# Kernel tuning notes

Hardware: AMD Instinct MI355X
Metric: run time of the kernel (lower is better)

Reference implementation:

```python
import jax, jax.numpy as jnp
import numpy as np

FL = 320       # frame length
FS = 80        # frame shift
ORDER = 16     # poly order (a[0] == 1)
EMPH = 0.97    # pre/de-emphasis coefficient


def setup_inputs() -> dict:
    key = jax.random.key(0)
    k1, k2 = jax.random.split(key)
    B, F = 64, 3000
    L = F * FS  # 240000
    excit = jax.random.normal(k1, (B, L, 1), dtype=jnp.float32) * 0.1
    # LPC coefficients: a[0] = 1, remaining taps small for numerical stability
    rest = jax.random.normal(k2, (B, F, ORDER - 1), dtype=jnp.float32) * (0.3 / (ORDER - 1))
    lpc_coef = jnp.concatenate([jnp.ones((B, F, 1), jnp.float32), rest], axis=-1)
    return {"excit": excit, "lpc_coef": lpc_coef}


def reference(excit, lpc_coef):
    """LPCSynthesisPytorch: AR synthesis recursion followed by de-emphasis.

    excit:    (B, L, 1)
    lpc_coef: (B, F, order), a[0] assumed 1, L = F * FS
    returns:  (B, L, 1)
    """
    B, L, _ = excit.shape
    order = lpc_coef.shape[-1]

    # Per-sample AR taps a[1:], expanded frame->sample, time-major for scan.
    a = jnp.repeat(lpc_coef[:, :, 1:], FS, axis=1)[:, :L]      # (B, L, order-1)
    a_t = jnp.transpose(a, (1, 0, 2))                          # (L, B, order-1)
    e_t = jnp.transpose(excit[..., 0], (1, 0))                 # (L, B)

    def ar_step(buf, inp):
        # buf: (B, order-1) = [x[n-order+1], ..., x[n-1]] (last entry most recent)
        a_n, e_n = inp
        # predicted = sum_k a[k] * x[n-k]; output = excit - predicted
        pre = -jnp.sum(a_n * buf[:, ::-1], axis=-1)
        out = e_n + pre
        buf = jnp.concatenate([buf[:, 1:], out[:, None]], axis=-1)
        return buf, out

    buf0 = jnp.zeros((B, order - 1), dtype=excit.dtype)
    _, y_t = jax.lax.scan(ar_step, buf0, (a_t, e_t))           # (L, B)

    # De-emphasis IIR: z[n] = y[n] + EMPH * z[n-1], z[-1] = 0
    def deemph_step(prev, x):
        cur = x + EMPH * prev
        return cur, cur

    _, z_t = jax.lax.scan(deemph_step, jnp.zeros((B,), excit.dtype), y_t)
    return jnp.transpose(z_t, (1, 0))[..., None]               # (B, L, 1)
```

## Files before the change

### kernel.cpp

```cpp
#include <hip/hip_runtime.h>


namespace {
constexpr int kFS = 80;
constexpr int kHS = 40;
constexpr int kF = 3000;
constexpr int kH = 2 * kF;
constexpr int kL = kFS * kF;
constexpr int kOrder = 16;
constexpr int kB = 64;
constexpr float kEmph = 0.97f;
constexpr int kThreads = 128;
constexpr int kJunk = 9;
constexpr int kEmitH = kThreads - kJunk;
constexpr int kSlotF = 44;
constexpr int kBufF = kThreads * kSlotF;
constexpr int kIss = kBufF / (2 * 64 * 4);
constexpr int kNT = 3;
constexpr int kCols = 17;
constexpr float kLg97 = -4.3943347e-2f;
constexpr float kR1 = 0.2957118f;
constexpr float kR2 = 0.08744547f;
constexpr float kR3 = 0.02585867f;
constexpr float kR4 = 0.00764671f;
constexpr float kR5 = 0.00226126f;
constexpr float kR6 = 6.6867e-4f;
constexpr float kR7 = 1.9773e-4f;
constexpr float kR8 = 5.8472e-5f;

typedef float vfloat4 __attribute__((ext_vector_type(4)));

__device__ __forceinline__ void stage_tile(const float* __restrict__ ebase,
                                           float* sbuf, int tile, int wv,
                                           int ln) {
#pragma unroll
  for (int i = 0; i < kIss; ++i) {
    const int c = wv * kIss + i;
    const int W4 = c * 64 + ln;
    const int s = W4 / 11;
    const int o4 = W4 - s * 11;
    const int ht = tile * kEmitH + s - kJunk;
    const int hc = min(max(ht, 0), kH - 1);
    const int fidx = min(hc * kHS + o4 * 4, kL - 4);
    __builtin_amdgcn_global_load_lds(
        (const __attribute__((address_space(1))) float*)(ebase + fidx),
        (__attribute__((address_space(3))) float*)(sbuf + (c << 8)), 16, 0,
        0);
  }
}
}

#define AR_SAMPLE(A, s, e_in, ACC)                                         \
  float ACC;                                                               \
  {                                                                        \
    float t0 = (e_in);                                                     \
    t0 = fmaf(-A[14], x[((s)-15) & 15], t0);                               \
    t0 = fmaf(-A[13], x[((s)-14) & 15], t0);                               \
    t0 = fmaf(-A[12], x[((s)-13) & 15], t0);                               \
    t0 = fmaf(-A[11], x[((s)-12) & 15], t0);                               \
    t0 = fmaf(-A[10], x[((s)-11) & 15], t0);                               \
    float t1 = -A[9] * x[((s)-10) & 15];                                   \
    t1 = fmaf(-A[8], x[((s)-9) & 15], t1);                                 \
    t1 = fmaf(-A[7], x[((s)-8) & 15], t1);                                 \
    t1 = fmaf(-A[6], x[((s)-7) & 15], t1);                                 \
    t1 = fmaf(-A[5], x[((s)-6) & 15], t1);                                 \
    float t2 = -A[4] * x[((s)-5) & 15];                                    \
    t2 = fmaf(-A[3], x[((s)-4) & 15], t2);                                 \
    t2 = fmaf(-A[2], x[((s)-3) & 15], t2);                                 \
    t2 = fmaf(-A[1], x[((s)-2) & 15], t2);                                 \
    const float t01 = t0 + t1;                      \
    t2 = fmaf(-A[0], x[((s)-1) & 15], t2);            \
    ACC = t01 + t2;                                           \
    x[(s)&15] = ACC;                                                       \
  }

__global__ __launch_bounds__(kThreads) void lpc_synth_kernel(
    const float* __restrict__ excit, const float* __restrict__ coef,
    float* __restrict__ out) {
  __shared__ float s_ex[2 * kBufF];
  __shared__ float s_zend[kThreads];
  __shared__ float s_zp[kThreads];

  const int tid = threadIdx.x;
  const int ln = tid & 63;
  const int wv = tid >> 6;
  const int b = blockIdx.y;
  const int tile0 = blockIdx.x * kNT;

  const float* __restrict__ ebase = excit + (size_t)b * kL;
  const float* __restrict__ cbase = coef + (size_t)b * kF * kOrder;
  float* __restrict__ outb = out + (size_t)b * kL;

  stage_tile(ebase, s_ex, tile0, wv, ln);

#pragma unroll 1
  for (int t = 0; t < kNT; ++t) {
    const int tile = tile0 + t;
    float* __restrict__ sb = s_ex + (t & 1) * kBufF;
    float* __restrict__ sn = s_ex + ((t + 1) & 1) * kBufF;

    __syncthreads();

    if (t + 1 < kNT) {
      stage_tile(ebase, sn, tile + 1, wv, ln);
      __builtin_amdgcn_sched_barrier(0);
    }

    const int ht = tile * kEmitH + tid - kJunk;
    const int hc = min(max(ht, 0), kH - 1);
    const int hw = min(max(ht - 2, 0), kH - 1);

    const vfloat4* __restrict__ cp_ =
        (const vfloat4*)(cbase + (size_t)(hw >> 1) * kOrder);
    const vfloat4* __restrict__ cc_ =
        (const vfloat4*)(cbase + (size_t)(hc >> 1) * kOrder);
    const vfloat4 p0 = cp_[0], p1 = cp_[1], p2 = cp_[2], p3 = cp_[3];
    const vfloat4 q0 = cc_[0], q1 = cc_[1], q2 = cc_[2], q3 = cc_[3];

    float x[16];
#pragma unroll
    for (int i = 0; i < 16; ++i) x[i] = 0.f;
    float pa_[15] = {p0.y, p0.z, p0.w, p1.x, p1.y, p1.z, p1.w, p2.x,
                     p2.y, p2.z, p2.w, p3.x, p3.y, p3.z, p3.w};
    const float ca_[15] = {q0.y, q0.z, q0.w, q1.x, q1.y, q1.z, q1.w, q2.x,
                           q2.y, q2.z, q2.w, q3.x, q3.y, q3.z, q3.w};
    {
      const float* __restrict__ s2 = sb + max(tid - 2, 0) * kSlotF;
      const float* __restrict__ s1 = sb + max(tid - 1, 0) * kSlotF;
      const float m2 = (ht >= 2) ? 1.f : 0.f;
      const float m1 = (ht >= 1) ? 1.f : 0.f;
#pragma unroll
      for (int j = 8; j < 10; ++j) {
        const vfloat4 v = *(const vfloat4*)(s2 + 4 * j);
        const float f_[4] = {m2 * v.x, m2 * v.y, m2 * v.z, m2 * v.w};
#pragma unroll
        for (int q = 0; q < 4; ++q) {
          AR_SAMPLE(pa_, 4 * (j - 8) + q, f_[q], acc)
          (void)acc;
        }
      }
      if (ht & 1) {
#pragma unroll
        for (int k = 0; k < 15; ++k) pa_[k] = ca_[k];
      }
#pragma unroll
      for (int j = 0; j < 10; ++j) {
        const vfloat4 v = *(const vfloat4*)(s1 + 4 * j);
        const float f_[4] = {m1 * v.x, m1 * v.y, m1 * v.z, m1 * v.w};
#pragma unroll
        for (int q = 0; q < 4; ++q) {
          AR_SAMPLE(pa_, 8 + 4 * j + q, f_[q], acc)
          (void)acc;
        }
      }
    }
    __syncthreads();

    float z = 0.f;
    {
      float* __restrict__ so = sb + tid * kSlotF;
#pragma unroll
      for (int j = 0; j < 10; ++j) {
        const vfloat4 v = *(const vfloat4*)(so + 4 * j);
        vfloat4 zv;
#pragma unroll
        for (int q = 0; q < 4; ++q) {
          AR_SAMPLE(ca_, 48 + 4 * j + q, v[q], acc)
          z = fmaf(kEmph, z, acc);
          if (q == 0) zv.x = z;
          if (q == 1) zv.y = z;
          if (q == 2) zv.z = z;
          if (q == 3) zv.w = z;
        }
        *(vfloat4*)(so + 4 * j) = zv;
      }
    }
    s_zend[tid] = (ht < 0 || ht >= kH) ? 0.f : z;
    __syncthreads();

    if (tid < kEmitH) {
      float Zp = s_zend[tid + 8];
      Zp = fmaf(kR1, s_zend[tid + 7], Zp);
      Zp = fmaf(kR2, s_zend[tid + 6], Zp);
      Zp = fmaf(kR3, s_zend[tid + 5], Zp);
      Zp = fmaf(kR4, s_zend[tid + 4], Zp);
      Zp = fmaf(kR5, s_zend[tid + 3], Zp);
      Zp = fmaf(kR6, s_zend[tid + 2], Zp);
      Zp = fmaf(kR7, s_zend[tid + 1], Zp);
      Zp = fmaf(kR8, s_zend[tid + 0], Zp);
      s_zp[tid] = Zp;
    }
    __syncthreads();

    {
      const int hbase = tile * kEmitH;
      const int nv4 = min(kEmitH, kH - hbase) * 10;
      vfloat4* __restrict__ ob = (vfloat4*)(outb + (size_t)hbase * kHS);
#pragma unroll 1
      for (int i = tid; i < nv4; i += kThreads) {
        const int k = i / 10;
        const int j = i - 10 * k;
        const vfloat4 h =
            *(const vfloat4*)(sb + (k + kJunk) * kSlotF + 4 * j);
        const float Zp = s_zp[k];
        const float ee = __builtin_exp2f(kLg97 * (float)(4 * j + 1));
        vfloat4 v;
        v.x = fmaf(ee, Zp, h.x);
        v.y = fmaf(ee * 0.97f, Zp, h.y);
        v.z = fmaf(ee * 0.9409f, Zp, h.z);
        v.w = fmaf(ee * 0.912673f, Zp, h.w);
        ob[i] = v;
      }
    }
  }
}
#undef AR_SAMPLE

extern "C" void kernel_launch(void* const* d_in, const int* in_sizes, int n_in,
                              void* d_out, int out_size, void* d_ws,
                              size_t ws_size, hipStream_t stream) {
  const float* excit = (const float*)d_in[0];
  const float* coef = (const float*)d_in[1];
  float* out = (float*)d_out;

  dim3 grid(kCols, kB);
  lpc_synth_kernel<<<grid, kThreads, 0, stream>>>(excit, coef, out);
}
```

Before: 139.5 us.

## Drop LDS staging and multi-tile loop; read excitation directly from global

Removes the double-buffered global_load_lds staging of excitation and the three-tile-per-block loop. Each thread now loads its own half-frames straight from global memory (three overlapping reads per thread), and the grid is tripled so each block processes one tile. LDS shrinks to a z-only buffer with a 42-float slot, accessed with float2 ops. This trades the async prefetch overlap for more blocks, higher occupancy and fewer barriers, at the cost of redundant global reads that rely on the cache.

```diff
diff --git a/kernel.cpp b/kernel.cpp
--- a/kernel.cpp
+++ b/kernel.cpp
@@ -2,22 +2,18 @@
 
 
 namespace {
-constexpr int kFS = 80;
 constexpr int kHS = 40;
 constexpr int kF = 3000;
 constexpr int kH = 2 * kF;
-constexpr int kL = kFS * kF;
+constexpr int kL = kHS * kH;
 constexpr int kOrder = 16;
 constexpr int kB = 64;
 constexpr float kEmph = 0.97f;
 constexpr int kThreads = 128;
 constexpr int kJunk = 9;
 constexpr int kEmitH = kThreads - kJunk;
-constexpr int kSlotF = 44;
-constexpr int kBufF = kThreads * kSlotF;
-constexpr int kIss = kBufF / (2 * 64 * 4);
-constexpr int kNT = 3;
-constexpr int kCols = 17;
+constexpr int kSlotF = 42;
+constexpr int kCols = 51;
 constexpr float kLg97 = -4.3943347e-2f;
 constexpr float kR1 = 0.2957118f;
 constexpr float kR2 = 0.08744547f;
@@ -29,25 +25,7 @@
 constexpr float kR8 = 5.8472e-5f;
 
 typedef float vfloat4 __attribute__((ext_vector_type(4)));
-
-__device__ __forceinline__ void stage_tile(const float* __restrict__ ebase,
-                                           float* sbuf, int tile, int wv,
-                                           int ln) {
-#pragma unroll
-  for (int i = 0; i < kIss; ++i) {
-    const int c = wv * kIss + i;
-    const int W4 = c * 64 + ln;
-    const int s = W4 / 11;
-    const int o4 = W4 - s * 11;
-    const int ht = tile * kEmitH + s - kJunk;
-    const int hc = min(max(ht, 0), kH - 1);
-    const int fidx = min(hc * kHS + o4 * 4, kL - 4);
-    __builtin_amdgcn_global_load_lds(
-        (const __attribute__((address_space(1))) float*)(ebase + fidx),
-        (__attribute__((address_space(3))) float*)(sbuf + (c << 8)), 16, 0,
-        0);
-  }
-}
+typedef float vfloat2 __attribute__((ext_vector_type(2)));
 }
 
 #define AR_SAMPLE(A, s, e_in, ACC)                                         \
@@ -77,140 +55,125 @@
 __global__ __launch_bounds__(kThreads) void lpc_synth_kernel(
     const float* __restrict__ excit, const float* __restrict__ coef,
     float* __restrict__ out) {
-  __shared__ float s_ex[2 * kBufF];
+  __shared__ float s_z[kThreads * kSlotF];
   __shared__ float s_zend[kThreads];
   __shared__ float s_zp[kThreads];
 
   const int tid = threadIdx.x;
-  const int ln = tid & 63;
-  const int wv = tid >> 6;
   const int b = blockIdx.y;
-  const int tile0 = blockIdx.x * kNT;
+  const int hbase = blockIdx.x * kEmitH;
+  const int ht = hbase + tid - kJunk;
+  const int hc = min(max(ht, 0), kH - 1);
+  const int h1 = min(max(ht - 1, 0), kH - 1);
+  const int h2 = min(max(ht - 2, 0), kH - 1);
 
   const float* __restrict__ ebase = excit + (size_t)b * kL;
   const float* __restrict__ cbase = coef + (size_t)b * kF * kOrder;
-  float* __restrict__ outb = out + (size_t)b * kL;
 
-  stage_tile(ebase, s_ex, tile0, wv, ln);
+  const vfloat4* __restrict__ cp_ =
+      (const vfloat4*)(cbase + (size_t)(h2 >> 1) * kOrder);
+  const vfloat4* __restrict__ cc_ =
+      (const vfloat4*)(cbase + (size_t)(hc >> 1) * kOrder);
+  const vfloat4 p0 = cp_[0], p1 = cp_[1], p2 = cp_[2], p3 = cp_[3];
+  const vfloat4 q0 = cc_[0], q1 = cc_[1], q2 = cc_[2], q3 = cc_[3];
 
-#pragma unroll 1
-  for (int t = 0; t < kNT; ++t) {
-    const int tile = tile0 + t;
-    float* __restrict__ sb = s_ex + (t & 1) * kBufF;
-    float* __restrict__ sn = s_ex + ((t + 1) & 1) * kBufF;
+  float pa_[15] = {p0.y, p0.z, p0.w, p1.x, p1.y, p1.z, p1.w, p2.x,
+                   p2.y, p2.z, p2.w, p3.x, p3.y, p3.z, p3.w};
+  const float ca_[15] = {q0.y, q0.z, q0.w, q1.x, q1.y, q1.z, q1.w, q2.x,
+                         q2.y, q2.z, q2.w, q3.x, q3.y, q3.z, q3.w};
 
-    __syncthreads();
+  float x[16];
+#pragma unroll
+  for (int i = 0; i < 16; ++i) x[i] = 0.f;
 
-    if (t + 1 < kNT) {
-      stage_tile(ebase, sn, tile + 1, wv, ln);
-      __builtin_amdgcn_sched_barrier(0);
-    }
-
-    const int ht = tile * kEmitH + tid - kJunk;
-    const int hc = min(max(ht, 0), kH - 1);
-    const int hw = min(max(ht - 2, 0), kH - 1);
-
-    const vfloat4* __restrict__ cp_ =
-        (const vfloat4*)(cbase + (size_t)(hw >> 1) * kOrder);
-    const vfloat4* __restrict__ cc_ =
-        (const vfloat4*)(cbase + (size_t)(hc >> 1) * kOrder);
-    const vfloat4 p0 = cp_[0], p1 = cp_[1], p2 = cp_[2], p3 = cp_[3];
-    const vfloat4 q0 = cc_[0], q1 = cc_[1], q2 = cc_[2], q3 = cc_[3];
-
-    float x[16];
+  {
+    const vfloat4* __restrict__ e2 = (const vfloat4*)(ebase + h2 * kHS);
+    const vfloat4* __restrict__ e1 = (const vfloat4*)(ebase + h1 * kHS);
+    const float m2 = (ht >= 2) ? 1.f : 0.f;
+    const float m1 = (ht >= 1) ? 1.f : 0.f;
 #pragma unroll
-    for (int i = 0; i < 16; ++i) x[i] = 0.f;
-    float pa_[15] = {p0.y, p0.z, p0.w, p1.x, p1.y, p1.z, p1.w, p2.x,
-                     p2.y, p2.z, p2.w, p3.x, p3.y, p3.z, p3.w};
-    const float ca_[15] = {q0.y, q0.z, q0.w, q1.x, q1.y, q1.z, q1.w, q2.x,
-                           q2.y, q2.z, q2.w, q3.x, q3.y, q3.z, q3.w};
-    {
-      const float* __restrict__ s2 = sb + max(tid - 2, 0) * kSlotF;
-      const float* __restrict__ s1 = sb + max(tid - 1, 0) * kSlotF;
-      const float m2 = (ht >= 2) ? 1.f : 0.f;
-      const float m1 = (ht >= 1) ? 1.f : 0.f;
+    for (int j = 8; j < 10; ++j) {
+      const vfloat4 v = e2[j];
+      const float f_[4] = {m2 * v.x, m2 * v.y, m2 * v.z, m2 * v.w};
 #pragma unroll
-      for (int j = 8; j < 10; ++j) {
-        const vfloat4 v = *(const vfloat4*)(s2 + 4 * j);
-        const float f_[4] = {m2 * v.x, m2 * v.y, m2 * v.z, m2 * v.w};
-#pragma unroll
-        for (int q = 0; q < 4; ++q) {
-          AR_SAMPLE(pa_, 4 * (j - 8) + q, f_[q], acc)
-          (void)acc;
-        }
-      }
-      if (ht & 1) {
-#pragma unroll
-        for (int k = 0; k < 15; ++k) pa_[k] = ca_[k];
-      }
-#pragma unroll
-      for (int j = 0; j < 10; ++j) {
-        const vfloat4 v = *(const vfloat4*)(s1 + 4 * j);
-        const float f_[4] = {m1 * v.x, m1 * v.y, m1 * v.z, m1 * v.w};
-#pragma unroll
-        for (int q = 0; q < 4; ++q) {
-          AR_SAMPLE(pa_, 8 + 4 * j + q, f_[q], acc)
-          (void)acc;
-        }
+      for (int q = 0; q < 4; ++q) {
+        AR_SAMPLE(pa_, 4 * (j - 8) + q, f_[q], acc)
+        (void)acc;
       }
     }
-    __syncthreads();
-
-    float z = 0.f;
-    {
-      float* __restrict__ so = sb + tid * kSlotF;
+    if (ht & 1) {
 #pragma unroll
-      for (int j = 0; j < 10; ++j) {
-        const vfloat4 v = *(const vfloat4*)(so + 4 * j);
-        vfloat4 zv;
+      for (int k = 0; k < 15; ++k) pa_[k] = ca_[k];
+    }
 #pragma unroll
-        for (int q = 0; q < 4; ++q) {
-          AR_SAMPLE(ca_, 48 + 4 * j + q, v[q], acc)
-          z = fmaf(kEmph, z, acc);
-          if (q == 0) zv.x = z;
-          if (q == 1) zv.y = z;
-          if (q == 2) zv.z = z;
-          if (q == 3) zv.w = z;
-        }
-        *(vfloat4*)(so + 4 * j) = zv;
+    for (int j = 0; j < 10; ++j) {
+      const vfloat4 v = e1[j];
+      const float f_[4] = {m1 * v.x, m1 * v.y, m1 * v.z, m1 * v.w};
+#pragma unroll
+      for (int q = 0; q < 4; ++q) {
+        AR_SAMPLE(pa_, 8 + 4 * j + q, f_[q], acc)
+        (void)acc;
       }
     }
-    s_zend[tid] = (ht < 0 || ht >= kH) ? 0.f : z;
-    __syncthreads();
+  }
 
-    if (tid < kEmitH) {
-      float Zp = s_zend[tid + 8];
-      Zp = fmaf(kR1, s_zend[tid + 7], Zp);
-      Zp = fmaf(kR2, s_zend[tid + 6], Zp);
-      Zp = fmaf(kR3, s_zend[tid + 5], Zp);
-      Zp = fmaf(kR4, s_zend[tid + 4], Zp);
-      Zp = fmaf(kR5, s_zend[tid + 3], Zp);
-      Zp = fmaf(kR6, s_zend[tid + 2], Zp);
-      Zp = fmaf(kR7, s_zend[tid + 1], Zp);
-      Zp = fmaf(kR8, s_zend[tid + 0], Zp);
-      s_zp[tid] = Zp;
+  float z = 0.f;
+  {
+    const vfloat4* __restrict__ ee_ = (const vfloat4*)(ebase + hc * kHS);
+    float* __restrict__ so = s_z + tid * kSlotF;
+#pragma unroll
+    for (int j = 0; j < 10; ++j) {
+      const vfloat4 v = ee_[j];
+      float zv[4];
+#pragma unroll
+      for (int q = 0; q < 4; ++q) {
+        AR_SAMPLE(ca_, 48 + 4 * j + q, v[q], acc)
+        z = fmaf(kEmph, z, acc);
+        zv[q] = z;
+      }
+      vfloat2 a, c;
+      a.x = zv[0]; a.y = zv[1];
+      c.x = zv[2]; c.y = zv[3];
+      *(vfloat2*)(so + 4 * j) = a;
+      *(vfloat2*)(so + 4 * j + 2) = c;
     }
-    __syncthreads();
+  }
+  s_zend[tid] = (ht < 0 || ht >= kH) ? 0.f : z;
+  __syncthreads();
 
-    {
-      const int hbase = tile * kEmitH;
-      const int nv4 = min(kEmitH, kH - hbase) * 10;
-      vfloat4* __restrict__ ob = (vfloat4*)(outb + (size_t)hbase * kHS);
+  if (tid < kEmitH) {
+    float Zp = s_zend[tid + 8];
+    Zp = fmaf(kR1, s_zend[tid + 7], Zp);
+    Zp = fmaf(kR2, s_zend[tid + 6], Zp);
+    Zp = fmaf(kR3, s_zend[tid + 5], Zp);
+    Zp = fmaf(kR4, s_zend[tid + 4], Zp);
+    Zp = fmaf(kR5, s_zend[tid + 3], Zp);
+    Zp = fmaf(kR6, s_zend[tid + 2], Zp);
+    Zp = fmaf(kR7, s_zend[tid + 1], Zp);
+    Zp = fmaf(kR8, s_zend[tid + 0], Zp);
+    s_zp[tid] = Zp;
+  }
+  __syncthreads();
+
+  {
+    const int nv4 = min(kEmitH, kH - hbase) * 10;
+    vfloat4* __restrict__ ob =
+        (vfloat4*)(out + (size_t)b * kL + (size_t)hbase * kHS);
 #pragma unroll 1
-      for (int i = tid; i < nv4; i += kThreads) {
-        const int k = i / 10;
-        const int j = i - 10 * k;
-        const vfloat4 h =
-            *(const vfloat4*)(sb + (k + kJunk) * kSlotF + 4 * j);
-        const float Zp = s_zp[k];
-        const float ee = __builtin_exp2f(kLg97 * (float)(4 * j + 1));
-        vfloat4 v;
-        v.x = fmaf(ee, Zp, h.x);
-        v.y = fmaf(ee * 0.97f, Zp, h.y);
-        v.z = fmaf(ee * 0.9409f, Zp, h.z);
-        v.w = fmaf(ee * 0.912673f, Zp, h.w);
-        ob[i] = v;
-      }
+    for (int i = tid; i < nv4; i += kThreads) {
+      const int k = i / 10;
+      const int j = i - 10 * k;
+      const float* sp = s_z + (k + kJunk) * kSlotF + 4 * j;
+      const vfloat2 h0 = *(const vfloat2*)sp;
+      const vfloat2 h1v = *(const vfloat2*)(sp + 2);
+      const float Zp = s_zp[k];
+      const float ee = __builtin_exp2f(kLg97 * (float)(4 * j + 1));
+      vfloat4 v;
+      v.x = fmaf(ee, Zp, h0.x);
+      v.y = fmaf(ee * 0.97f, Zp, h0.y);
+      v.z = fmaf(ee * 0.9409f, Zp, h1v.x);
+      v.w = fmaf(ee * 0.912673f, Zp, h1v.y);
+      ob[i] = v;
     }
   }
 }
```

Result: no change. 136.8 us (-1.9%).
